# Kernel tuning notes

Hardware: AMD Instinct MI355X
Metric: run time of the kernel (lower is better)

## Reference

```python
import jax, jax.numpy as jnp
import numpy as np

N_JOINTS = 21
N_DIMS = 3


def setup_inputs() -> dict:
    key = jax.random.key(0)
    k1, k2 = jax.random.split(key)
    B = 262144
    pred = jax.random.normal(k1, (B, N_JOINTS * N_DIMS), dtype=jnp.float32)
    target = jax.random.normal(k2, (B, N_JOINTS * N_DIMS), dtype=jnp.float32)
    return {"pred": pred, "target": target}


def reference(pred, target):
    # [B, 63] -> [B, 21, 3]; per-joint Euclidean distance, then mean over
    # joints and batch (mean-of-means over equal-sized groups == global mean).
    B = pred.shape[0]
    diff = pred.reshape(B, N_JOINTS, N_DIMS) - target.reshape(B, N_JOINTS, N_DIMS)
    dist = jnp.sqrt(jnp.sum(diff * diff, axis=-1))  # [B, 21]
    return jnp.mean(dist)
```

## Files before the change

kernel.cpp:

```cpp
#include <hip/hip_runtime.h>

#define NBLOCKS 1024
#define NTHREADS 256

__device__ __forceinline__ float wave_reduce(float v) {
    #pragma unroll
    for (int off = 32; off > 0; off >>= 1) v += __shfl_down(v, off, 64);
    return v;
}

__global__ __launch_bounds__(NTHREADS) void dis_partial_kernel(
    const float* __restrict__ pred, const float* __restrict__ targ,
    float* __restrict__ partials, int nquad, int ntrip) {
    const int tid = blockIdx.x * NTHREADS + threadIdx.x;
    const int stride = gridDim.x * NTHREADS;
    float acc = 0.f;

    const float4* p4 = (const float4*)pred;
    const float4* t4 = (const float4*)targ;

    for (int i = tid; i < nquad; i += stride) {
        float4 pa = p4[3 * i + 0];
        float4 pb = p4[3 * i + 1];
        float4 pc = p4[3 * i + 2];
        float4 ta = t4[3 * i + 0];
        float4 tb = t4[3 * i + 1];
        float4 tc = t4[3 * i + 2];

        float dx, dy, dz;
        dx = pa.x - ta.x; dy = pa.y - ta.y; dz = pa.z - ta.z;
        acc += sqrtf(dx * dx + dy * dy + dz * dz);
        dx = pa.w - ta.w; dy = pb.x - tb.x; dz = pb.y - tb.y;
        acc += sqrtf(dx * dx + dy * dy + dz * dz);
        dx = pb.z - tb.z; dy = pb.w - tb.w; dz = pc.x - tc.x;
        acc += sqrtf(dx * dx + dy * dy + dz * dz);
        dx = pc.y - tc.y; dy = pc.z - tc.z; dz = pc.w - tc.w;
        acc += sqrtf(dx * dx + dy * dy + dz * dz);
    }

    for (int j = 4 * nquad + tid; j < ntrip; j += stride) {
        float dx = pred[3 * j + 0] - targ[3 * j + 0];
        float dy = pred[3 * j + 1] - targ[3 * j + 1];
        float dz = pred[3 * j + 2] - targ[3 * j + 2];
        acc += sqrtf(dx * dx + dy * dy + dz * dz);
    }

    acc = wave_reduce(acc);

    __shared__ float smem[NTHREADS / 64];
    const int lane = threadIdx.x & 63;
    const int wave = threadIdx.x >> 6;
    if (lane == 0) smem[wave] = acc;
    __syncthreads();
    if (threadIdx.x == 0) {
        float s = 0.f;
        #pragma unroll
        for (int w = 0; w < NTHREADS / 64; ++w) s += smem[w];
        partials[blockIdx.x] = s;
    }
}

__global__ __launch_bounds__(NTHREADS) void dis_finalize_kernel(
    const float* __restrict__ partials, float* __restrict__ out,
    int nblocks, float scale) {
    float acc = 0.f;
    for (int i = threadIdx.x; i < nblocks; i += NTHREADS) acc += partials[i];
    acc = wave_reduce(acc);

    __shared__ float smem[NTHREADS / 64];
    const int lane = threadIdx.x & 63;
    const int wave = threadIdx.x >> 6;
    if (lane == 0) smem[wave] = acc;
    __syncthreads();
    if (threadIdx.x == 0) {
        float s = 0.f;
        #pragma unroll
        for (int w = 0; w < NTHREADS / 64; ++w) s += smem[w];
        out[0] = s * scale;
    }
}

extern "C" void kernel_launch(void* const* d_in, const int* in_sizes, int n_in,
                              void* d_out, int out_size, void* d_ws, size_t ws_size,
                              hipStream_t stream) {
    const float* pred = (const float*)d_in[0];
    const float* targ = (const float*)d_in[1];
    float* out = (float*)d_out;
    float* partials = (float*)d_ws;

    const int n = in_sizes[0];
    const int ntrip = n / 3;
    const int nquad = n / 12;
    const float scale = 1.0f / (float)ntrip;

    dis_partial_kernel<<<NBLOCKS, NTHREADS, 0, stream>>>(pred, targ, partials,
                                                         nquad, ntrip);
    dis_finalize_kernel<<<1, NTHREADS, 0, stream>>>(partials, out, NBLOCKS, scale);
}
```

Measured before the change: 144.2 us.

## Stage coalesced float4 differences through LDS tiles before per-joint distance

Replaces the per-thread strided 3x float4 loads (each thread reading 48 contiguous bytes, leaving gaps between lanes) with fully coalesced float4 loads per block tile. The differences go to shared memory, and each thread then reads xyz triples from LDS. The grid also grows from 1024 to 1792 blocks. This costs two barriers per tile and LDS traffic with stride-3 access, which may add bank pressure, in exchange for cleaner global memory coalescing in a bandwidth-bound reduction.

```diff
diff --git a/kernel.cpp b/kernel.cpp
--- a/kernel.cpp
+++ b/kernel.cpp
@@ -1,7 +1,10 @@
 #include <hip/hip_runtime.h>
 
-#define NBLOCKS 1024
 #define NTHREADS 256
+#define NBLOCKS 1792
+#define TILE_F4 768
+#define TILE_FLOATS 3072
+#define TILE_TRIPLES 1024
 
 __device__ __forceinline__ float wave_reduce(float v) {
     #pragma unroll
@@ -9,55 +12,62 @@
     return v;
 }
 
+__device__ __forceinline__ float block_reduce(float v) {
+    v = wave_reduce(v);
+    __shared__ float smem[NTHREADS / 64];
+    const int lane = threadIdx.x & 63;
+    const int wave = threadIdx.x >> 6;
+    if (lane == 0) smem[wave] = v;
+    __syncthreads();
+    float s = 0.f;
+    if (threadIdx.x == 0) {
+        #pragma unroll
+        for (int w = 0; w < NTHREADS / 64; ++w) s += smem[w];
+    }
+    return s;
+}
+
 __global__ __launch_bounds__(NTHREADS) void dis_partial_kernel(
+    const float4* __restrict__ p4, const float4* __restrict__ t4,
     const float* __restrict__ pred, const float* __restrict__ targ,
-    float* __restrict__ partials, int nquad, int ntrip) {
-    const int tid = blockIdx.x * NTHREADS + threadIdx.x;
-    const int stride = gridDim.x * NTHREADS;
+    float* __restrict__ partials, int ntile, int ntrip) {
+    __shared__ float diff[TILE_FLOATS];
+    const int t = threadIdx.x;
     float acc = 0.f;
 
-    const float4* p4 = (const float4*)pred;
-    const float4* t4 = (const float4*)targ;
+    for (int tile = blockIdx.x; tile < ntile; tile += gridDim.x) {
+        const int base = tile * TILE_F4;
+        #pragma unroll
+        for (int j = 0; j < 3; ++j) {
+            const int idx = base + j * NTHREADS + t;
+            float4 p = p4[idx];
+            float4 q = t4[idx];
+            float4 d;
+            d.x = p.x - q.x; d.y = p.y - q.y; d.z = p.z - q.z; d.w = p.w - q.w;
+            ((float4*)diff)[j * NTHREADS + t] = d;
+        }
+        __syncthreads();
+        #pragma unroll
+        for (int j = 0; j < 4; ++j) {
+            const int tr = j * NTHREADS + t;
+            const float dx = diff[3 * tr + 0];
+            const float dy = diff[3 * tr + 1];
+            const float dz = diff[3 * tr + 2];
+            acc += sqrtf(dx * dx + dy * dy + dz * dz);
+        }
+        __syncthreads();
+    }
 
-    for (int i = tid; i < nquad; i += stride) {
-        float4 pa = p4[3 * i + 0];
-        float4 pb = p4[3 * i + 1];
-        float4 pc = p4[3 * i + 2];
-        float4 ta = t4[3 * i + 0];
-        float4 tb = t4[3 * i + 1];
-        float4 tc = t4[3 * i + 2];
-
-        float dx, dy, dz;
-        dx = pa.x - ta.x; dy = pa.y - ta.y; dz = pa.z - ta.z;
-        acc += sqrtf(dx * dx + dy * dy + dz * dz);
-        dx = pa.w - ta.w; dy = pb.x - tb.x; dz = pb.y - tb.y;
-        acc += sqrtf(dx * dx + dy * dy + dz * dz);
-        dx = pb.z - tb.z; dy = pb.w - tb.w; dz = pc.x - tc.x;
-        acc += sqrtf(dx * dx + dy * dy + dz * dz);
-        dx = pc.y - tc.y; dy = pc.z - tc.z; dz = pc.w - tc.w;
+    for (int j = ntile * TILE_TRIPLES + blockIdx.x * NTHREADS + t; j < ntrip;
+         j += gridDim.x * NTHREADS) {
+        const float dx = pred[3 * j + 0] - targ[3 * j + 0];
+        const float dy = pred[3 * j + 1] - targ[3 * j + 1];
+        const float dz = pred[3 * j + 2] - targ[3 * j + 2];
         acc += sqrtf(dx * dx + dy * dy + dz * dz);
     }
 
-    for (int j = 4 * nquad + tid; j < ntrip; j += stride) {
-        float dx = pred[3 * j + 0] - targ[3 * j + 0];
-        float dy = pred[3 * j + 1] - targ[3 * j + 1];
-        float dz = pred[3 * j + 2] - targ[3 * j + 2];
-        acc += sqrtf(dx * dx + dy * dy + dz * dz);
-    }
-
-    acc = wave_reduce(acc);
-
-    __shared__ float smem[NTHREADS / 64];
-    const int lane = threadIdx.x & 63;
-    const int wave = threadIdx.x >> 6;
-    if (lane == 0) smem[wave] = acc;
-    __syncthreads();
-    if (threadIdx.x == 0) {
-        float s = 0.f;
-        #pragma unroll
-        for (int w = 0; w < NTHREADS / 64; ++w) s += smem[w];
-        partials[blockIdx.x] = s;
-    }
+    const float s = block_reduce(acc);
+    if (threadIdx.x == 0) partials[blockIdx.x] = s;
 }
 
 __global__ __launch_bounds__(NTHREADS) void dis_finalize_kernel(
@@ -65,19 +75,8 @@
     int nblocks, float scale) {
     float acc = 0.f;
     for (int i = threadIdx.x; i < nblocks; i += NTHREADS) acc += partials[i];
-    acc = wave_reduce(acc);
-
-    __shared__ float smem[NTHREADS / 64];
-    const int lane = threadIdx.x & 63;
-    const int wave = threadIdx.x >> 6;
-    if (lane == 0) smem[wave] = acc;
-    __syncthreads();
-    if (threadIdx.x == 0) {
-        float s = 0.f;
-        #pragma unroll
-        for (int w = 0; w < NTHREADS / 64; ++w) s += smem[w];
-        out[0] = s * scale;
-    }
+    const float s = block_reduce(acc);
+    if (threadIdx.x == 0) out[0] = s * scale;
 }
 
 extern "C" void kernel_launch(void* const* d_in, const int* in_sizes, int n_in,
@@ -90,10 +89,10 @@
 
     const int n = in_sizes[0];
     const int ntrip = n / 3;
-    const int nquad = n / 12;
+    const int ntile = n / TILE_FLOATS;
     const float scale = 1.0f / (float)ntrip;
 
-    dis_partial_kernel<<<NBLOCKS, NTHREADS, 0, stream>>>(pred, targ, partials,
-                                                         nquad, ntrip);
+    dis_partial_kernel<<<NBLOCKS, NTHREADS, 0, stream>>>(
+        (const float4*)pred, (const float4*)targ, pred, targ, partials, ntile, ntrip);
     dis_finalize_kernel<<<1, NTHREADS, 0, stream>>>(partials, out, NBLOCKS, scale);
 }
```

Result: no change. 143.2 us (-0.7%).
